# Kernel tuning notes

Hardware: AMD Instinct MI355X
Metric: run time of the kernel (lower is better)

## Reference

```python
import jax, jax.numpy as jnp
import numpy as np

D = 1024   # 'heads' arg = d_model
H = 4      # no_of_heads
DH = D // H
B, T = 4, 2048


def _ln(x, g, b, eps=1e-5):
    m = x.mean(-1, keepdims=True)
    v = ((x - m) ** 2).mean(-1, keepdims=True)
    return (x - m) / jnp.sqrt(v + eps) * g + b


def _heads_proj(x, W):
    # x: [B,T,D]; W: [H,dh,dh] per-head nn.Linear weights (out = x @ W^T)
    b, t, c = x.shape
    h, dh, _ = W.shape
    xh = x.reshape(b, t, h, dh)  # channel slices i*dh:(i+1)*dh == reshape
    return jnp.einsum('bthd,hed->bthe', xh, W)


def _self_attn(x, wq, wk, wv, masked):
    q = _heads_proj(x, wq)
    k = _heads_proj(x, wk)
    v = _heads_proj(x, wv)
    dh = wq.shape[-1]
    s = jnp.einsum('bthe,bshe->bhts', q, k) * dh ** -0.5  # [B,H,T,T]
    if masked:
        t = x.shape[1]
        causal = jnp.tril(jnp.ones((t, t), dtype=bool))
        s = jnp.where(causal, s, -jnp.inf)
    a = jax.nn.softmax(s, axis=-1)
    o = jnp.einsum('bhts,bshd->bthd', a, v)
    return o.reshape(x.shape)


def _cross_attn(ctx, x, wq, wk, wv):
    # NOTE: the original CrossAttention applies NO softmax — faithful copy.
    q = _heads_proj(x, wq)
    k = _heads_proj(ctx, wk)
    v = _heads_proj(ctx, wv)
    dh = wq.shape[-1]
    s = jnp.einsum('bthe,bshe->bhts', q, k) * dh ** -0.5
    o = jnp.einsum('bhts,bshd->bthd', s, v)
    return o.reshape(x.shape)


def _ffn(x, w1, b1, w2, b2):
    return jax.nn.relu(x @ w1.T + b1) @ w2.T + b2


def setup_inputs() -> dict:
    key = jax.random.key(0)
    ks = jax.random.split(key, 16)
    sc = 0.02
    d = {
        'context': jax.random.normal(ks[0], (B, T, D), jnp.float32),
        'X': jax.random.normal(ks[1], (B, T, D), jnp.float32),
        'dec_wq': jax.random.normal(ks[2], (H, DH, DH), jnp.float32) * sc,
        'dec_wk': jax.random.normal(ks[3], (H, DH, DH), jnp.float32) * sc,
        'dec_wv': jax.random.normal(ks[4], (H, DH, DH), jnp.float32) * sc,
        'x_wq': jax.random.normal(ks[5], (H, DH, DH), jnp.float32) * sc,
        'x_wk': jax.random.normal(ks[6], (H, DH, DH), jnp.float32) * sc,
        'x_wv': jax.random.normal(ks[7], (H, DH, DH), jnp.float32) * sc,
        'enc_wq': jax.random.normal(ks[8], (H, DH, DH), jnp.float32) * sc,
        'enc_wk': jax.random.normal(ks[9], (H, DH, DH), jnp.float32) * sc,
        'enc_wv': jax.random.normal(ks[10], (H, DH, DH), jnp.float32) * sc,
        'dec_w1': jax.random.normal(ks[11], (4 * D, D), jnp.float32) * sc,
        'dec_b1': jnp.zeros((4 * D,), jnp.float32),
        'dec_w2': jax.random.normal(ks[12], (D, 4 * D), jnp.float32) * sc,
        'dec_b2': jnp.zeros((D,), jnp.float32),
        'enc_w1': jax.random.normal(ks[13], (4 * D, D), jnp.float32) * sc,
        'enc_b1': jnp.zeros((4 * D,), jnp.float32),
        'enc_w2': jax.random.normal(ks[14], (D, 4 * D), jnp.float32) * sc,
        'enc_b2': jnp.zeros((D,), jnp.float32),
        'dec_ln1_g': jnp.ones((D,), jnp.float32), 'dec_ln1_b': jnp.zeros((D,), jnp.float32),
        'dec_ln2_g': jnp.ones((D,), jnp.float32), 'dec_ln2_b': jnp.zeros((D,), jnp.float32),
        'dec_ln3_g': jnp.ones((D,), jnp.float32), 'dec_ln3_b': jnp.zeros((D,), jnp.float32),
        'enc_ln1_g': jnp.ones((D,), jnp.float32), 'enc_ln1_b': jnp.zeros((D,), jnp.float32),
        'enc_ln2_g': jnp.ones((D,), jnp.float32), 'enc_ln2_b': jnp.zeros((D,), jnp.float32),
    }
    return d


def reference(context, X, dec_wq, dec_wk, dec_wv, x_wq, x_wk, x_wv,
              enc_wq, enc_wk, enc_wv, dec_w1, dec_b1, dec_w2, dec_b2,
              enc_w1, enc_b1, enc_w2, enc_b2,
              dec_ln1_g, dec_ln1_b, dec_ln2_g, dec_ln2_b, dec_ln3_g, dec_ln3_b,
              enc_ln1_g, enc_ln1_b, enc_ln2_g, enc_ln2_b):
    # Dropout (p=0.1) treated as identity (eval mode).
    x1 = _ln(X + _self_attn(X, dec_wq, dec_wk, dec_wv, True), dec_ln1_g, dec_ln1_b)
    # EncoderBlock on context (non-masked self-attn + FFN)
    c = _ln(context + _self_attn(context, enc_wq, enc_wk, enc_wv, False), enc_ln1_g, enc_ln1_b)
    c = _ln(c + _ffn(c, enc_w1, enc_b1, enc_w2, enc_b2), enc_ln2_g, enc_ln2_b)
    x2 = _ln(x1 + _cross_attn(c, x1, x_wq, x_wk, x_wv), dec_ln2_g, dec_ln2_b)
    out = _ln(x2 + _ffn(x2, dec_w1, dec_b1, dec_w2, dec_b2), dec_ln3_g, dec_ln3_b)
    return (c, out)
```

## Files before the change

### kernel.cpp

```cpp
#include <hip/hip_runtime.h>
#include <hip/hip_bf16.h>

typedef unsigned short u16;
typedef __bf16 bf16x8 __attribute__((ext_vector_type(8)));
typedef unsigned short u16x8 __attribute__((ext_vector_type(8)));
typedef unsigned short u16x4 __attribute__((ext_vector_type(4)));
typedef float f32x4 __attribute__((ext_vector_type(4)));

#define DI static __device__ __forceinline__

DI u16 f2bf(float f) {
    unsigned u = __builtin_bit_cast(unsigned, f);
    u += 0x7FFFu + ((u >> 16) & 1u);
    return (u16)(u >> 16);
}
DI float bf2f(u16 u) {
    unsigned x = ((unsigned)u) << 16;
    return __builtin_bit_cast(float, x);
}
DI u16x8 ld8_f32(const float* __restrict__ p) {
    const float4 a = *(const float4*)p;
    const float4 b = *(const float4*)(p + 4);
    u16x8 r = { f2bf(a.x), f2bf(a.y), f2bf(a.z), f2bf(a.w),
                f2bf(b.x), f2bf(b.y), f2bf(b.z), f2bf(b.w) };
    return r;
}
DI f32x4 mfma16(u16x8 a, u16x8 b, f32x4 c) {
    return __builtin_amdgcn_mfma_f32_16x16x32_bf16(
        __builtin_bit_cast(bf16x8, a), __builtin_bit_cast(bf16x8, b), c, 0, 0, 0);
}

__global__ void __launch_bounds__(256) k_cast(const float* __restrict__ in,
                                              u16* __restrict__ out, long n4) {
    long i = (long)blockIdx.x * 256 + threadIdx.x;
    if (i >= n4) return;
    const float4 v = *(const float4*)(in + i * 4);
    u16x4 o = { f2bf(v.x), f2bf(v.y), f2bf(v.z), f2bf(v.w) };
    *(u16x4*)(out + i * 4) = o;
}

template <int AF32, int BF32>
__global__ void __launch_bounds__(256, 2) k_gemm_bt(
    const void* __restrict__ Ap, long lda,
    const void* __restrict__ Bp, long ldb,
    float* __restrict__ Cf, u16* __restrict__ Cb, long ldc,
    const float* __restrict__ bias, int relu, int accum, float alpha, int K,
    int Hdiv, long sAb, long sAh, long sBb, long sBh, long sCb, long sCh)
{
    __shared__ __align__(16) u16 As[128 * 72];
    __shared__ __align__(16) u16 Bs[128 * 72];
    const int tid  = threadIdx.x;
    const int lane = tid & 63, wave = tid >> 6;
    const int r16  = lane & 15, quad = lane >> 4;
    const int wr   = (wave >> 1) * 64, wc = (wave & 1) * 64;
    const int zb = blockIdx.z / Hdiv, zh = blockIdx.z % Hdiv;
    const long aoff = (long)zb * sAb + (long)zh * sAh + (long)blockIdx.x * 128 * lda;
    const long boff = (long)zb * sBb + (long)zh * sBh + (long)blockIdx.y * 128 * ldb;
    const u16*   A16 = (const u16*)Ap + aoff;
    const float* A32 = (const float*)Ap + aoff;
    const u16*   B16 = (const u16*)Bp + boff;
    const float* B32 = (const float*)Bp + boff;
    const long coff = (long)zb * sCb + (long)zh * sCh +
                      (long)blockIdx.x * 128 * ldc + (long)blockIdx.y * 128;

    f32x4 acc[4][4];
#pragma unroll
    for (int i = 0; i < 4; i++)
#pragma unroll
        for (int j = 0; j < 4; j++) acc[i][j] = f32x4{0.f, 0.f, 0.f, 0.f};

    const int st_row = tid >> 3;
    const int st_col = (tid & 7) * 8;

    u16x8 ar0, ar1, ar2, ar3, br0, br1, br2, br3;

#define LDAB(KS)                                                              \
    do {                                                                      \
        const long kk0_ = (long)(KS) * 64 + st_col;                           \
        if constexpr (AF32) {                                                 \
            ar0 = ld8_f32(A32 + (long)(st_row)      * lda + kk0_);            \
            ar1 = ld8_f32(A32 + (long)(st_row + 32) * lda + kk0_);            \
            ar2 = ld8_f32(A32 + (long)(st_row + 64) * lda + kk0_);            \
            ar3 = ld8_f32(A32 + (long)(st_row + 96) * lda + kk0_);            \
        } else {                                                              \
            ar0 = *(const u16x8*)(A16 + (long)(st_row)      * lda + kk0_);    \
            ar1 = *(const u16x8*)(A16 + (long)(st_row + 32) * lda + kk0_);    \
            ar2 = *(const u16x8*)(A16 + (long)(st_row + 64) * lda + kk0_);    \
            ar3 = *(const u16x8*)(A16 + (long)(st_row + 96) * lda + kk0_);    \
        }                                                                     \
        if constexpr (BF32) {                                                 \
            br0 = ld8_f32(B32 + (long)(st_row)      * ldb + kk0_);            \
            br1 = ld8_f32(B32 + (long)(st_row + 32) * ldb + kk0_);            \
            br2 = ld8_f32(B32 + (long)(st_row + 64) * ldb + kk0_);            \
            br3 = ld8_f32(B32 + (long)(st_row + 96) * ldb + kk0_);            \
        } else {                                                              \
            br0 = *(const u16x8*)(B16 + (long)(st_row)      * ldb + kk0_);    \
            br1 = *(const u16x8*)(B16 + (long)(st_row + 32) * ldb + kk0_);    \
            br2 = *(const u16x8*)(B16 + (long)(st_row + 64) * ldb + kk0_);    \
            br3 = *(const u16x8*)(B16 + (long)(st_row + 96) * ldb + kk0_);    \
        }                                                                     \
    } while (0)

#define STAB()                                                                \
    do {                                                                      \
        u16* ap_ = As + st_row * 72 + st_col;                                 \
        *(u16x8*)(ap_)            = ar0;                                      \
        *(u16x8*)(ap_ + 32 * 72)  = ar1;                                      \
        *(u16x8*)(ap_ + 64 * 72)  = ar2;                                      \
        *(u16x8*)(ap_ + 96 * 72)  = ar3;                                      \
        u16* bp_ = Bs + st_row * 72 + st_col;                                 \
        *(u16x8*)(bp_)            = br0;                                      \
        *(u16x8*)(bp_ + 32 * 72)  = br1;                                      \
        *(u16x8*)(bp_ + 64 * 72)  = br2;                                      \
        *(u16x8*)(bp_ + 96 * 72)  = br3;                                      \
    } while (0)

    LDAB(0);
    STAB();
    __syncthreads();

    const int nks = K >> 6;
    for (int ks = 0; ks < nks; ks++) {
        const bool more = (ks + 1 < nks);
        if (more) LDAB(ks + 1);
#pragma unroll
        for (int kk = 0; kk < 64; kk += 32) {
            u16x8 af[4], bfr[4];
#pragma unroll
            for (int i = 0; i < 4; i++)
                af[i] = *(const u16x8*)(As + (wr + i * 16 + r16) * 72 + kk + 8 * quad);
#pragma unroll
            for (int j = 0; j < 4; j++)
                bfr[j] = *(const u16x8*)(Bs + (wc + j * 16 + r16) * 72 + kk + 8 * quad);
#pragma unroll
            for (int i = 0; i < 4; i++)
#pragma unroll
                for (int j = 0; j < 4; j++)
                    acc[i][j] = mfma16(af[i], bfr[j], acc[i][j]);
        }
        __syncthreads();
        if (more) {
            STAB();
            __syncthreads();
        }
    }
#undef LDAB
#undef STAB

#pragma unroll
    for (int i = 0; i < 4; i++) {
#pragma unroll
        for (int j = 0; j < 4; j++) {
            const int gcol = wc + j * 16 + r16;
            const float bv = bias ? bias[blockIdx.y * 128 + gcol] : 0.f;
#pragma unroll
            for (int r = 0; r < 4; r++) {
                const long o = coff + (long)(wr + i * 16 + quad * 4 + r) * ldc + gcol;
                float v = acc[i][j][r] * alpha + bv;
                if (accum) v += Cf[o];
                if (relu) v = fmaxf(v, 0.f);
                if (Cf) Cf[o] = v;
                if (Cb) Cb[o] = f2bf(v);
            }
        }
    }
}

template <int NSEG>
__global__ void __launch_bounds__(256) k_proj(
    const float* __restrict__ A,
    const float* __restrict__ W0, const float* __restrict__ W1,
    const float* __restrict__ W2,
    u16* __restrict__ C0, u16* __restrict__ C1, u16* __restrict__ C2)
{
    __shared__ __align__(16) u16 As[128 * 72];
    __shared__ __align__(16) u16 Bs[128 * 72];
    const int tid  = threadIdx.x;
    const int lane = tid & 63, wave = tid >> 6;
    const int r16  = lane & 15, quad = lane >> 4;
    const int wr   = (wave >> 1) * 64, wc = (wave & 1) * 64;
    const int seg = blockIdx.y >> 1, yy = blockIdx.y & 1, h = blockIdx.z;
    const float* W = (NSEG >= 3 && seg == 2) ? W2 : (seg == 1 ? W1 : W0);
    u16*         C = (NSEG >= 3 && seg == 2) ? C2 : (seg == 1 ? C1 : C0);
    const float* Ab = A + (long)blockIdx.x * 128 * 1024 + h * 256;
    const float* Bb = W + (long)h * 65536 + yy * 128 * 256;
    u16* Cp = C + (long)blockIdx.x * 128 * 1024 + h * 256 + yy * 128;

    f32x4 acc[4][4];
#pragma unroll
    for (int i = 0; i < 4; i++)
#pragma unroll
        for (int j = 0; j < 4; j++) acc[i][j] = f32x4{0.f, 0.f, 0.f, 0.f};

    const int st_row = tid >> 3, st_col = (tid & 7) * 8;

    for (int k0 = 0; k0 < 256; k0 += 64) {
#pragma unroll
        for (int r = 0; r < 4; r++) {
            const int row = st_row + 32 * r;
            *(u16x8*)(As + row * 72 + st_col) = ld8_f32(Ab + (long)row * 1024 + k0 + st_col);
            *(u16x8*)(Bs + row * 72 + st_col) = ld8_f32(Bb + (long)row * 256 + k0 + st_col);
        }
        __syncthreads();
#pragma unroll
        for (int kk = 0; kk < 64; kk += 32) {
            u16x8 af[4], bfr[4];
#pragma unroll
            for (int i = 0; i < 4; i++)
                af[i] = *(const u16x8*)(As + (wr + i * 16 + r16) * 72 + kk + 8 * quad);
#pragma unroll
            for (int j = 0; j < 4; j++)
                bfr[j] = *(const u16x8*)(Bs + (wc + j * 16 + r16) * 72 + kk + 8 * quad);
#pragma unroll
            for (int i = 0; i < 4; i++)
#pragma unroll
                for (int j = 0; j < 4; j++)
                    acc[i][j] = mfma16(af[i], bfr[j], acc[i][j]);
        }
        __syncthreads();
    }

#pragma unroll
    for (int i = 0; i < 4; i++)
#pragma unroll
        for (int j = 0; j < 4; j++)
#pragma unroll
            for (int r = 0; r < 4; r++)
                Cp[(long)(wr + i * 16 + quad * 4 + r) * 1024 + wc + j * 16 + r16] =
                    f2bf(acc[i][j][r]);
}

template <int MASKED>
__global__ void __launch_bounds__(512, 2) k_attn(
    const u16* __restrict__ Q, const u16* __restrict__ Kg, const u16* __restrict__ Vt,
    u16* __restrict__ O, int T, float scale)
{
    const int D = 1024;
    __shared__ __align__(16) u16 Ks[2][64 * 264];
    __shared__ __align__(16) u16 VsT[2][256 * 72];
    __shared__ __align__(16) u16 Ps[8][16 * 72];
    const int tid = threadIdx.x, lane = tid & 63, wave = tid >> 6;
    const int r16 = lane & 15, quad = lane >> 4;

    const int fid = blockIdx.x;
    const int swz = ((fid & 7) << 5) | (fid >> 3);
    const int grp = swz & 15, hh = (swz >> 4) & 3, bb = swz >> 6;

    int qr0, nkb, myMax;
    if (MASKED) {
        const int strip = (wave < 4) ? grp : (31 - grp);
        qr0   = strip * 64 + (wave & 3) * 16;
        myMax = strip;
        nkb   = 32 - grp;
    } else {
        qr0   = grp * 128 + wave * 16;
        myMax = 1 << 30;
        nkb   = T / 64;
    }

    const long base   = ((long)bb * T) * D + hh * 256;
    const long vtbase = ((long)(bb * 4 + hh) * 256) * 2048;

    u16x8 qf[8];
#pragma unroll
    for (int ks = 0; ks < 8; ks++)
        qf[ks] = *(const u16x8*)(Q + base + (long)(qr0 + r16) * D + ks * 32 + 8 * quad);

    f32x4 oacc[16];
#pragma unroll
    for (int nt = 0; nt < 16; nt++) oacc[nt] = f32x4{0.f, 0.f, 0.f, 0.f};
    f32x4 lacc = f32x4{0.f, 0.f, 0.f, 0.f};
    const u16x8 ones8 = {0x3F80, 0x3F80, 0x3F80, 0x3F80,
                         0x3F80, 0x3F80, 0x3F80, 0x3F80};

    const int krow = tid >> 5, kcol = (tid & 31) * 8;
    const int vrow = tid >> 3, vcol = (tid & 7) * 8;

    const u16* kg = Kg + base;
    const u16* vg = Vt + vtbase + (long)vrow * 2048 + vcol;

    uint4 kr0, kr1, kr2, kr3, vr0, vr1, vr2, vr3;

#define LD_KV(KB)                                                          \
    do {                                                                   \
        const u16* kp_ = kg + ((long)(KB) * 64 + krow) * D + kcol;         \
        kr0 = *(const uint4*)(kp_);                                        \
        kr1 = *(const uint4*)(kp_ + 16 * D);                               \
        kr2 = *(const uint4*)(kp_ + 32 * D);                               \
        kr3 = *(const uint4*)(kp_ + 48 * D);                               \
        const u16* vp_ = vg + (KB) * 64;                                   \
        vr0 = *(const uint4*)(vp_);                                        \
        vr1 = *(const uint4*)(vp_ + 64 * 2048);                            \
        vr2 = *(const uint4*)(vp_ + 128 * 2048);                           \
        vr3 = *(const uint4*)(vp_ + 192 * 2048);                           \
    } while (0)

#define ST_KV(P)                                                           \
    do {                                                                   \
        u16* kq_ = Ks[P] + krow * 264 + kcol;                              \
        *(uint4*)(kq_)            = kr0;                                   \
        *(uint4*)(kq_ + 16 * 264) = kr1;                                   \
        *(uint4*)(kq_ + 32 * 264) = kr2;                                   \
        *(uint4*)(kq_ + 48 * 264) = kr3;                                   \
        u16* vq_ = VsT[P] + vrow * 72 + vcol;                              \
        *(uint4*)(vq_)            = vr0;                                   \
        *(uint4*)(vq_ + 64 * 72)  = vr1;                                   \
        *(uint4*)(vq_ + 128 * 72) = vr2;                                   \
        *(uint4*)(vq_ + 192 * 72) = vr3;                                   \
    } while (0)

    LD_KV(0);
    ST_KV(0);
    __syncthreads();

    u16* const pw = &Ps[wave][0];
    int p = 0;

    for (int kb = 0; kb < nkb; kb++) {
        const bool more = (kb + 1 < nkb);
        if (more) LD_KV(kb + 1);

        if (!MASKED || kb <= myMax) {
            const u16* ks_ = Ks[p];
            const u16* vs_ = VsT[p];

            f32x4 s0 = f32x4{0.f,0.f,0.f,0.f}, s1 = f32x4{0.f,0.f,0.f,0.f};
            f32x4 s2 = f32x4{0.f,0.f,0.f,0.f}, s3 = f32x4{0.f,0.f,0.f,0.f};
            __builtin_amdgcn_s_setprio(1);
#pragma unroll
            for (int ks = 0; ks < 8; ks++) {
                const u16x8 a = qf[ks];
                const u16* kp = ks_ + r16 * 264 + ks * 32 + 8 * quad;
                s0 = mfma16(a, *(const u16x8*)(kp),            s0);
                s1 = mfma16(a, *(const u16x8*)(kp + 16 * 264), s1);
                s2 = mfma16(a, *(const u16x8*)(kp + 32 * 264), s2);
                s3 = mfma16(a, *(const u16x8*)(kp + 48 * 264), s3);
            }
            __builtin_amdgcn_s_setprio(0);

            const bool domask = MASKED && (kb == myMax);

#pragma unroll
            for (int r = 0; r < 4; r++) {
                float a0 = s0[r] * scale, a1 = s1[r] * scale;
                float a2 = s2[r] * scale, a3 = s3[r] * scale;
                if (domask) {
                    const int qi = qr0 + quad * 4 + r;
                    const int kb0 = kb * 64;
                    if (kb0 + r16 > qi)      a0 = -1e30f;
                    if (kb0 + 16 + r16 > qi) a1 = -1e30f;
                    if (kb0 + 32 + r16 > qi) a2 = -1e30f;
                    if (kb0 + 48 + r16 > qi) a3 = -1e30f;
                }
                const float p0 = __expf(fminf(a0, 30.f));
                const float p1 = __expf(fminf(a1, 30.f));
                const float p2 = __expf(fminf(a2, 30.f));
                const float p3 = __expf(fminf(a3, 30.f));
                u16* pr = pw + (quad * 4 + r) * 72 + r16;
                pr[0]  = f2bf(p0);
                pr[16] = f2bf(p1);
                pr[32] = f2bf(p2);
                pr[48] = f2bf(p3);
            }

            const u16* pp = pw + r16 * 72 + 8 * quad;
            const u16x8 pfA = *(const u16x8*)(pp);
            const u16x8 pfB = *(const u16x8*)(pp + 32);
            __builtin_amdgcn_s_setprio(1);
            lacc = mfma16(pfA, ones8, lacc);
            lacc = mfma16(pfB, ones8, lacc);
#pragma unroll
            for (int nt = 0; nt < 16; nt++) {
                const u16* vp = vs_ + (nt * 16 + r16) * 72 + 8 * quad;
                oacc[nt] = mfma16(pfA, *(const u16x8*)(vp),      oacc[nt]);
                oacc[nt] = mfma16(pfB, *(const u16x8*)(vp + 32), oacc[nt]);
            }
            __builtin_amdgcn_s_setprio(0);
        }

        if (more) {
            ST_KV(p ^ 1);
            __syncthreads();
        }
        p ^= 1;
    }
#undef LD_KV
#undef ST_KV

#pragma unroll
    for (int r = 0; r < 4; r++) lacc[r] = 1.f / lacc[r];
#pragma unroll
    for (int nt = 0; nt < 16; nt++)
#pragma unroll
        for (int r = 0; r < 4; r++)
            O[base + (long)(qr0 + quad * 4 + r) * D + nt * 16 + r16] =
                f2bf(oacc[nt][r] * lacc[r]);
}

template <int XF32, int RF32>
__global__ void __launch_bounds__(256) k_addln(
    const void* __restrict__ Xp, const void* __restrict__ Rp,
    const float* __restrict__ G, const float* __restrict__ Bv,
    float* __restrict__ Yf, u16* __restrict__ Yb)
{
    const int tid = threadIdx.x;
    const long off = (long)blockIdx.x * 1024 + tid * 4;
    float v[4];
    if constexpr (XF32) {
        const float4 a = *(const float4*)((const float*)Xp + off);
        v[0] = a.x; v[1] = a.y; v[2] = a.z; v[3] = a.w;
    } else {
        const u16x4 a = *(const u16x4*)((const u16*)Xp + off);
        v[0] = bf2f(a[0]); v[1] = bf2f(a[1]); v[2] = bf2f(a[2]); v[3] = bf2f(a[3]);
    }
    if constexpr (RF32) {
        const float4 b = *(const float4*)((const float*)Rp + off);
        v[0] += b.x; v[1] += b.y; v[2] += b.z; v[3] += b.w;
    } else {
        const u16x4 b = *(const u16x4*)((const u16*)Rp + off);
        v[0] += bf2f(b[0]); v[1] += bf2f(b[1]); v[2] += bf2f(b[2]); v[3] += bf2f(b[3]);
    }
    float s1 = v[0] + v[1] + v[2] + v[3];
    float s2 = v[0]*v[0] + v[1]*v[1] + v[2]*v[2] + v[3]*v[3];
#pragma unroll
    for (int m = 1; m < 64; m <<= 1) { s1 += __shfl_xor(s1, m); s2 += __shfl_xor(s2, m); }
    __shared__ float red[8];
    if ((tid & 63) == 0) { red[(tid >> 6) * 2] = s1; red[(tid >> 6) * 2 + 1] = s2; }
    __syncthreads();
    s1 = red[0] + red[2] + red[4] + red[6];
    s2 = red[1] + red[3] + red[5] + red[7];
    const float mean = s1 * (1.f / 1024.f);
    const float rstd = rsqrtf(s2 * (1.f / 1024.f) - mean * mean + 1e-5f);
    const float4 g  = *(const float4*)(G + tid * 4);
    const float4 be = *(const float4*)(Bv + tid * 4);
    const float o0 = (v[0] - mean) * rstd * g.x + be.x;
    const float o1 = (v[1] - mean) * rstd * g.y + be.y;
    const float o2 = (v[2] - mean) * rstd * g.z + be.z;
    const float o3 = (v[3] - mean) * rstd * g.w + be.w;
    if (Yf) { float4 of = {o0, o1, o2, o3}; *(float4*)(Yf + off) = of; }
    if (Yb) { u16x4 ob = {f2bf(o0), f2bf(o1), f2bf(o2), f2bf(o3)}; *(u16x4*)(Yb + off) = ob; }
}

__global__ void __launch_bounds__(256) k_transpose(const u16* __restrict__ Xin,
                                                   u16* __restrict__ Y)
{
    __shared__ u16 tile[32][33];
    const int tx = threadIdx.x & 31, ty = threadIdx.x >> 5;
    const int t0 = blockIdx.x * 32, e0 = blockIdx.y * 32, bh = blockIdx.z;
    const int b = bh >> 2, h = bh & 3;
#pragma unroll
    for (int i = 0; i < 4; i++)
        tile[ty + 8 * i][tx] =
            Xin[((long)(b * 2048 + t0 + ty + 8 * i)) * 1024 + h * 256 + e0 + tx];
    __syncthreads();
#pragma unroll
    for (int i = 0; i < 4; i++)
        Y[((long)bh * 256 + e0 + ty + 8 * i) * 2048 + t0 + tx] = tile[tx][ty + 8 * i];
}

#define GEMM(AF, BF, Aptr, lda, Bptr, ldb, pCf, pCb, ldc, bias, relu, accum, alpha, \
             M, N, K, Z, Hdiv, sAb, sAh, sBb, sBh, sCb, sCh)                        \
    k_gemm_bt<AF, BF><<<dim3((M) / 128, (N) / 128, (Z)), dim3(256), 0, stream>>>(   \
        (const void*)(Aptr), (lda), (const void*)(Bptr), (ldb), (pCf), (pCb),       \
        (ldc), (bias), (relu), (accum), (alpha), (K), (Hdiv),                       \
        (long)(sAb), (long)(sAh), (long)(sBb), (long)(sBh), (long)(sCb), (long)(sCh))

extern "C" void kernel_launch(void* const* d_in, const int* in_sizes, int n_in,
                              void* d_out, int out_size, void* d_ws, size_t ws_size,
                              hipStream_t stream)
{
    const int Bn = 4, T = 2048, D = 1024, H = 4, DH = 256;
    const long BTD = (long)Bn * T * D;
    const long MB = 1024 * 1024;

    const float* ctx = (const float*)d_in[0];
    const float* X   = (const float*)d_in[1];
    const float* Wh[9]; for (int i = 0; i < 9; i++) Wh[i] = (const float*)d_in[2 + i];
    const float* dec_w1 = (const float*)d_in[11]; const float* dec_b1 = (const float*)d_in[12];
    const float* dec_w2 = (const float*)d_in[13]; const float* dec_b2 = (const float*)d_in[14];
    const float* enc_w1 = (const float*)d_in[15]; const float* enc_b1 = (const float*)d_in[16];
    const float* enc_w2 = (const float*)d_in[17]; const float* enc_b2 = (const float*)d_in[18];
    const float* ln[10]; for (int i = 0; i < 10; i++) ln[i] = (const float*)d_in[19 + i];
    (void)in_sizes; (void)n_in; (void)out_size; (void)ws_size;

    float* outC = (float*)d_out;
    float* outY = (float*)d_out + BTD;

    char* w = (char*)d_ws;
    u16*   qb   = (u16*)(w);
    u16*   kb   = (u16*)(w + 16 * MB);
    u16*   vb   = (u16*)(w + 32 * MB);
    u16*   tmpB = (u16*)(w + 48 * MB);
    u16*   hb64 = (u16*)(w);
    u16*   Kt2  = (u16*)(w + 32 * MB);
    u16*   crossO= (u16*)(w + 32 * MB);
    u16*   Vt2  = (u16*)(w + 48 * MB);
    u16*   Nm   = (u16*)(w + 64 * MB);
    u16*   x1b  = (u16*)(w + 66 * MB);
    u16*   t2b  = (u16*)(w + 82 * MB);

    u16* w1o = (u16*)outY;
    u16* w2o = w1o + 4194304;
    u16* foutE = w1o + 8388608;
    u16* foutD = x1b;

    k_proj<3><<<dim3(64, 6, 4), dim3(256), 0, stream>>>(
        X, Wh[0], Wh[1], Wh[2], qb, kb, vb);
    k_transpose<<<dim3(T / 32, DH / 32, Bn * H), dim3(256), 0, stream>>>(vb, tmpB);
    k_attn<1><<<dim3(256), dim3(512), 0, stream>>>(qb, kb, tmpB, vb, T, 0.0625f);
    k_addln<1, 0><<<dim3(Bn * T), dim3(256), 0, stream>>>(X, vb, ln[0], ln[1], nullptr, x1b);

    k_proj<3><<<dim3(64, 6, 4), dim3(256), 0, stream>>>(
        ctx, Wh[6], Wh[7], Wh[8], qb, kb, vb);
    k_transpose<<<dim3(T / 32, DH / 32, Bn * H), dim3(256), 0, stream>>>(vb, tmpB);
    k_attn<0><<<dim3(256), dim3(512), 0, stream>>>(qb, kb, tmpB, vb, T, 0.0625f);
    k_addln<1, 0><<<dim3(Bn * T), dim3(256), 0, stream>>>(ctx, vb, ln[6], ln[7], nullptr, t2b);

    k_cast<<<dim3(4096), dim3(256), 0, stream>>>(enc_w1, w1o, 1048576);
    k_cast<<<dim3(4096), dim3(256), 0, stream>>>(enc_w2, w2o, 1048576);
    GEMM(0, 0, t2b, D, w1o, D, nullptr, hb64, 4096, enc_b1, 1, 0, 1.f,
         Bn * T, 4096, 1024, 1, 1, 0, 0, 0, 0, 0, 0);
    GEMM(0, 0, hb64, 4096, w2o, 4096, nullptr, foutE, 1024, enc_b2, 0, 0, 1.f,
         Bn * T, 1024, 4096, 1, 1, 0, 0, 0, 0, 0, 0);
    k_addln<0, 0><<<dim3(Bn * T), dim3(256), 0, stream>>>(
        t2b, foutE, ln[8], ln[9], outC, nullptr);

    GEMM(0, 1, x1b, D, Wh[3], DH, nullptr, qb, D, nullptr, 0, 0, 1.f,
         Bn * T, DH, DH, H, H, 0, DH, 0, DH * DH, 0, DH);
    k_proj<2><<<dim3(64, 4, 4), dim3(256), 0, stream>>>(
        outC, Wh[4], Wh[5], nullptr, kb, t2b, nullptr);
    k_transpose<<<dim3(T / 32, DH / 32, Bn * H), dim3(256), 0, stream>>>(kb, Kt2);
    k_transpose<<<dim3(T / 32, DH / 32, Bn * H), dim3(256), 0, stream>>>(t2b, Vt2);
    GEMM(0, 0, Vt2, T, Kt2, T, nullptr, Nm, DH, nullptr, 0, 0, 1.f,
         DH, DH, T, Bn * H, Bn * H, 0, (long)DH * T, 0, (long)DH * T, 0, DH * DH);
    GEMM(0, 0, qb, D, Nm, DH, nullptr, crossO, D, nullptr, 0, 0, 0.0625f,
         T, DH, DH, Bn * H, H, (long)T * D, DH, (long)H * DH * DH, DH * DH,
         (long)T * D, DH);
    k_addln<0, 0><<<dim3(Bn * T), dim3(256), 0, stream>>>(x1b, crossO, ln[2], ln[3], nullptr, t2b);

    k_cast<<<dim3(4096), dim3(256), 0, stream>>>(dec_w1, w1o, 1048576);
    k_cast<<<dim3(4096), dim3(256), 0, stream>>>(dec_w2, w2o, 1048576);
    GEMM(0, 0, t2b, D, w1o, D, nullptr, hb64, 4096, dec_b1, 1, 0, 1.f,
         Bn * T, 4096, 1024, 1, 1, 0, 0, 0, 0, 0, 0);
    GEMM(0, 0, hb64, 4096, w2o, 4096, nullptr, foutD, 1024, dec_b2, 0, 0, 1.f,
         Bn * T, 1024, 4096, 1, 1, 0, 0, 0, 0, 0, 0);
    k_addln<0, 0><<<dim3(Bn * T), dim3(256), 0, stream>>>(
        t2b, foutD, ln[4], ln[5], outY, nullptr);
}
```

Measured before the change: 819.5 us.

## Add 256x128 bf16 GEMM for FFN up-projection, fuse transposes, overlap attention KV stores

Adds a 512-thread GEMM kernel with 256x128 tiles and uses it for both FFN first-layer GEMMs (bias plus ReLU, bf16 output). The larger tile gives more reuse per shared-memory load than the generic 128x128 kernel. The two cross-attention transposes become one launch through a dual-input transpose kernel. In the attention kernel, the next KV tile is now stored to shared memory before the PV MFMAs instead of after them, which overlaps LDS writes with compute. The new GEMM has no K-tail or bounds handling, and the larger tiles may lower occupancy.

```diff
diff --git a/kernel.cpp b/kernel.cpp
--- a/kernel.cpp
+++ b/kernel.cpp
@@ -166,6 +166,105 @@
     }
 }
 
+__global__ void __launch_bounds__(512, 2) k_gemm256(
+    const u16* __restrict__ A, long lda,
+    const u16* __restrict__ B, long ldb,
+    u16* __restrict__ Cb, long ldc,
+    const float* __restrict__ bias, int relu, int K)
+{
+    __shared__ __align__(16) u16 As[256 * 72];
+    __shared__ __align__(16) u16 Bs[128 * 72];
+    const int tid  = threadIdx.x;
+    const int lane = tid & 63, wave = tid >> 6;
+    const int r16  = lane & 15, quad = lane >> 4;
+    const int wr   = (wave >> 1) * 64, wc = (wave & 1) * 64;
+    const u16* Ab = A + (long)blockIdx.x * 256 * lda;
+    const u16* Bb = B + (long)blockIdx.y * 128 * ldb;
+    const long coff = (long)blockIdx.x * 256 * ldc + blockIdx.y * 128;
+
+    f32x4 acc[4][4];
+#pragma unroll
+    for (int i = 0; i < 4; i++)
+#pragma unroll
+        for (int j = 0; j < 4; j++) acc[i][j] = f32x4{0.f, 0.f, 0.f, 0.f};
+
+    const int st_row = tid >> 3;
+    const int st_col = (tid & 7) * 8;
+
+    u16x8 ar0, ar1, ar2, ar3, br0, br1;
+
+#define LDAB(KS)                                                              \
+    do {                                                                      \
+        const long kk0_ = (long)(KS) * 64 + st_col;                           \
+        ar0 = *(const u16x8*)(Ab + (long)(st_row)       * lda + kk0_);        \
+        ar1 = *(const u16x8*)(Ab + (long)(st_row + 64)  * lda + kk0_);        \
+        ar2 = *(const u16x8*)(Ab + (long)(st_row + 128) * lda + kk0_);        \
+        ar3 = *(const u16x8*)(Ab + (long)(st_row + 192) * lda + kk0_);        \
+        br0 = *(const u16x8*)(Bb + (long)(st_row)       * ldb + kk0_);        \
+        br1 = *(const u16x8*)(Bb + (long)(st_row + 64)  * ldb + kk0_);        \
+    } while (0)
+
+#define STAB()                                                                \
+    do {                                                                      \
+        u16* ap_ = As + st_row * 72 + st_col;                                 \
+        *(u16x8*)(ap_)             = ar0;                                     \
+        *(u16x8*)(ap_ + 64 * 72)   = ar1;                                     \
+        *(u16x8*)(ap_ + 128 * 72)  = ar2;                                     \
+        *(u16x8*)(ap_ + 192 * 72)  = ar3;                                     \
+        u16* bp_ = Bs + st_row * 72 + st_col;                                 \
+        *(u16x8*)(bp_)             = br0;                                     \
+        *(u16x8*)(bp_ + 64 * 72)   = br1;                                     \
+    } while (0)
+
+    LDAB(0);
+    STAB();
+    __syncthreads();
+
+    const int nks = K >> 6;
+    for (int ks = 0; ks < nks; ks++) {
+        const bool more = (ks + 1 < nks);
+        if (more) LDAB(ks + 1);
+#pragma unroll
+        for (int kk = 0; kk < 64; kk += 32) {
+            u16x8 af[4], bfr[4];
+#pragma unroll
+            for (int i = 0; i < 4; i++)
+                af[i] = *(const u16x8*)(As + (wr + i * 16 + r16) * 72 + kk + 8 * quad);
+#pragma unroll
+            for (int j = 0; j < 4; j++)
+                bfr[j] = *(const u16x8*)(Bs + (wc + j * 16 + r16) * 72 + kk + 8 * quad);
+#pragma unroll
+            for (int i = 0; i < 4; i++)
+#pragma unroll
+                for (int j = 0; j < 4; j++)
+                    acc[i][j] = mfma16(af[i], bfr[j], acc[i][j]);
+        }
+        __syncthreads();
+        if (more) {
+            STAB();
+            __syncthreads();
+        }
+    }
+#undef LDAB
+#undef STAB
+
+#pragma unroll
+    for (int i = 0; i < 4; i++) {
+#pragma unroll
+        for (int j = 0; j < 4; j++) {
+            const int gcol = wc + j * 16 + r16;
+            const float bv = bias ? bias[blockIdx.y * 128 + gcol] : 0.f;
+#pragma unroll
+            for (int r = 0; r < 4; r++) {
+                const long o = coff + (long)(wr + i * 16 + quad * 4 + r) * ldc + gcol;
+                float v = acc[i][j][r] + bv;
+                if (relu) v = fmaxf(v, 0.f);
+                Cb[o] = f2bf(v);
+            }
+        }
+    }
+}
+
 template <int NSEG>
 __global__ void __launch_bounds__(256) k_proj(
     const float* __restrict__ A,
@@ -363,6 +462,8 @@
                 pr[48] = f2bf(p3);
             }
 
+            if (more) ST_KV(p ^ 1);
+
             const u16* pp = pw + r16 * 72 + 8 * quad;
             const u16x8 pfA = *(const u16x8*)(pp);
             const u16x8 pfB = *(const u16x8*)(pp + 32);
@@ -376,12 +477,11 @@
                 oacc[nt] = mfma16(pfB, *(const u16x8*)(vp + 32), oacc[nt]);
             }
             __builtin_amdgcn_s_setprio(0);
-        }
-
-        if (more) {
+        } else if (more) {
             ST_KV(p ^ 1);
-            __syncthreads();
-        }
+        }
+
+        if (more) __syncthreads();
         p ^= 1;
     }
 #undef LD_KV
@@ -441,12 +541,17 @@
     if (Yb) { u16x4 ob = {f2bf(o0), f2bf(o1), f2bf(o2), f2bf(o3)}; *(u16x4*)(Yb + off) = ob; }
 }
 
-__global__ void __launch_bounds__(256) k_transpose(const u16* __restrict__ Xin,
-                                                   u16* __restrict__ Y)
+__global__ void __launch_bounds__(256) k_transpose2(
+    const u16* __restrict__ X0, u16* __restrict__ Y0,
+    const u16* __restrict__ X1, u16* __restrict__ Y1)
 {
     __shared__ u16 tile[32][33];
     const int tx = threadIdx.x & 31, ty = threadIdx.x >> 5;
-    const int t0 = blockIdx.x * 32, e0 = blockIdx.y * 32, bh = blockIdx.z;
+    const int zz = blockIdx.z;
+    const int bh = zz & 15;
+    const u16* Xin = (zz < 16) ? X0 : X1;
+    u16*       Y   = (zz < 16) ? Y0 : Y1;
+    const int t0 = blockIdx.x * 32, e0 = blockIdx.y * 32;
     const int b = bh >> 2, h = bh & 3;
 #pragma unroll
     for (int i = 0; i < 4; i++)
@@ -506,20 +611,22 @@
 
     k_proj<3><<<dim3(64, 6, 4), dim3(256), 0, stream>>>(
         X, Wh[0], Wh[1], Wh[2], qb, kb, vb);
-    k_transpose<<<dim3(T / 32, DH / 32, Bn * H), dim3(256), 0, stream>>>(vb, tmpB);
+    k_transpose2<<<dim3(T / 32, DH / 32, 16), dim3(256), 0, stream>>>(
+        vb, tmpB, nullptr, nullptr);
     k_attn<1><<<dim3(256), dim3(512), 0, stream>>>(qb, kb, tmpB, vb, T, 0.0625f);
     k_addln<1, 0><<<dim3(Bn * T), dim3(256), 0, stream>>>(X, vb, ln[0], ln[1], nullptr, x1b);
 
     k_proj<3><<<dim3(64, 6, 4), dim3(256), 0, stream>>>(
         ctx, Wh[6], Wh[7], Wh[8], qb, kb, vb);
-    k_transpose<<<dim3(T / 32, DH / 32, Bn * H), dim3(256), 0, stream>>>(vb, tmpB);
+    k_transpose2<<<dim3(T / 32, DH / 32, 16), dim3(256), 0, stream>>>(
+        vb, tmpB, nullptr, nullptr);
     k_attn<0><<<dim3(256), dim3(512), 0, stream>>>(qb, kb, tmpB, vb, T, 0.0625f);
     k_addln<1, 0><<<dim3(Bn * T), dim3(256), 0, stream>>>(ctx, vb, ln[6], ln[7], nullptr, t2b);
 
     k_cast<<<dim3(4096), dim3(256), 0, stream>>>(enc_w1, w1o, 1048576);
     k_cast<<<dim3(4096), dim3(256), 0, stream>>>(enc_w2, w2o, 1048576);
-    GEMM(0, 0, t2b, D, w1o, D, nullptr, hb64, 4096, enc_b1, 1, 0, 1.f,
-         Bn * T, 4096, 1024, 1, 1, 0, 0, 0, 0, 0, 0);
+    k_gemm256<<<dim3(32, 32), dim3(512), 0, stream>>>(
+        t2b, D, w1o, D, hb64, 4096, enc_b1, 1, 1024);
     GEMM(0, 0, hb64, 4096, w2o, 4096, nullptr, foutE, 1024, enc_b2, 0, 0, 1.f,
          Bn * T, 1024, 4096, 1, 1, 0, 0, 0, 0, 0, 0);
     k_addln<0, 0><<<dim3(Bn * T), dim3(256), 0, stream>>>(
@@ -529,8 +636,8 @@
          Bn * T, DH, DH, H, H, 0, DH, 0, DH * DH, 0, DH);
     k_proj<2><<<dim3(64, 4, 4), dim3(256), 0, stream>>>(
         outC, Wh[4], Wh[5], nullptr, kb, t2b, nullptr);
-    k_transpose<<<dim3(T / 32, DH / 32, Bn * H), dim3(256), 0, stream>>>(kb, Kt2);
-    k_transpose<<<dim3(T / 32, DH / 32, Bn * H), dim3(256), 0, stream>>>(t2b, Vt2);
+    k_transpose2<<<dim3(T / 32, DH / 32, 32), dim3(256), 0, stream>>>(
+        kb, Kt2, t2b, Vt2);
     GEMM(0, 0, Vt2, T, Kt2, T, nullptr, Nm, DH, nullptr, 0, 0, 1.f,
          DH, DH, T, Bn * H, Bn * H, 0, (long)DH * T, 0, (long)DH * T, 0, DH * DH);
     GEMM(0, 0, qb, D, Nm, DH, nullptr, crossO, D, nullptr, 0, 0, 0.0625f,
@@ -540,8 +647,8 @@
 
     k_cast<<<dim3(4096), dim3(256), 0, stream>>>(dec_w1, w1o, 1048576);
     k_cast<<<dim3(4096), dim3(256), 0, stream>>>(dec_w2, w2o, 1048576);
-    GEMM(0, 0, t2b, D, w1o, D, nullptr, hb64, 4096, dec_b1, 1, 0, 1.f,
-         Bn * T, 4096, 1024, 1, 1, 0, 0, 0, 0, 0, 0);
+    k_gemm256<<<dim3(32, 32), dim3(512), 0, stream>>>(
+        t2b, D, w1o, D, hb64, 4096, dec_b1, 1, 1024);
     GEMM(0, 0, hb64, 4096, w2o, 4096, nullptr, foutD, 1024, dec_b2, 0, 0, 1.f,
          Bn * T, 1024, 4096, 1, 1, 0, 0, 0, 0, 0, 0);
     k_addln<0, 0><<<dim3(Bn * T), dim3(256), 0, stream>>>(
```

Result: slower. 850.5 us (+3.8%).
